# Performance work log

Measured on AMD Instinct MI355X. Metric: run time of the kernel, lower is better.

The kernel has to match this reference:

```python
import jax, jax.numpy as jnp
import numpy as np

B, N, K, D, H, FF, L, NH = 8, 50, 20, 3, 128, 2048, 3, 8
S = N * K
HD = H // NH


def setup_inputs() -> dict:
    key = jax.random.key(0)
    ks = jax.random.split(key, 16)
    visited = jax.random.uniform(ks[0], (B, S)) < 0.05
    # the single most-recent action per batch row (status flips 0 -> 1)
    action_idx = jax.random.randint(ks[1], (B,), 0, S)
    visited = visited.at[jnp.arange(B), action_idx].set(True)
    feats = jax.random.normal(ks[2], (B, S, D - 1)) * visited[:, :, None]
    state = jnp.concatenate([feats, visited[:, :, None].astype(jnp.float32)], axis=-1)
    prev_state = state.at[jnp.arange(B), action_idx, :].set(0.0)

    def w(k, shape, s=0.02):
        return jax.random.normal(k, shape, dtype=jnp.float32) * s

    return dict(
        prev_state=prev_state, state=state,
        W_pre=w(ks[3], (D, H)), b_pre=jnp.zeros(H),
        Wq=w(ks[4], (L, H, H)), bq=jnp.zeros((L, H)),
        Wk=w(ks[5], (L, H, H)), bk=jnp.zeros((L, H)),
        Wv=w(ks[6], (L, H, H)), bv=jnp.zeros((L, H)),
        Wo=w(ks[7], (L, H, H)), bo=jnp.zeros((L, H)),
        ln1_g=jnp.ones((L, H)), ln1_b=jnp.zeros((L, H)),
        Wff1=w(ks[8], (L, H, FF)), bff1=jnp.zeros((L, FF)),
        Wff2=w(ks[9], (L, FF, H)), bff2=jnp.zeros((L, H)),
        ln2_g=jnp.ones((L, H)), ln2_b=jnp.zeros((L, H)),
        W_comb=w(ks[10], (2 * H, H)), b_comb=jnp.zeros(H),
        W_dec=w(ks[11], (H, H)), b_dec=jnp.zeros(H),
        W_lin=w(ks[12], (S, S)), b_lin=jnp.zeros(S),
    )


def _layer_norm(x, g, b, eps=1e-5):
    m = jnp.mean(x, -1, keepdims=True)
    v = jnp.mean(jnp.square(x - m), -1, keepdims=True)
    return (x - m) * jax.lax.rsqrt(v + eps) * g + b


def _update_mask(state):
    # vectorized equivalent of the original Python-loop scatter mask
    status = state[:, :, -1] != 0                      # visited [B, S], S = K*N channel-major
    mask = status
    vis_kn = status.reshape(B, K, N)
    user_any = vis_kn.any(axis=1)                      # [B, N]: user visited on any channel
    mask = mask | jnp.broadcast_to(user_any[:, None, :], (B, K, N)).reshape(B, S)
    assigned = state.reshape(B, K, N, D).sum(-1) != 0  # [B, K, N]
    full = assigned.sum(-1) >= 2                       # [B, K]: channel already has 2 users
    mask = mask | jnp.broadcast_to(full[:, :, None], (B, K, N)).reshape(B, S)
    return mask


def reference(prev_state, state, W_pre, b_pre, Wq, bq, Wk, bk, Wv, bv, Wo, bo,
              ln1_g, ln1_b, Wff1, bff1, Wff2, bff2, ln2_g, ln2_b,
              W_comb, b_comb, W_dec, b_dec, W_lin, b_lin):
    mask = _update_mask(state)
    # exactly one status change per batch row (sequential RL step)
    diff = prev_state[:, :, -1] != state[:, :, -1]
    act_idx = jnp.argmax(diff, axis=1)                 # [B]

    x = state @ W_pre + b_pre                          # [B, S, H]
    scale = np.float32(1.0 / np.sqrt(HD))
    for i in range(L):  # 3 post-LN transformer encoder layers
        q = (x @ Wq[i] + bq[i]).reshape(B, S, NH, HD)
        k = (x @ Wk[i] + bk[i]).reshape(B, S, NH, HD)
        v = (x @ Wv[i] + bv[i]).reshape(B, S, NH, HD)
        att = jax.nn.softmax(jnp.einsum('bqhd,bkhd->bhqk', q, k) * scale, axis=-1)
        o = jnp.einsum('bhqk,bkhd->bqhd', att, v).reshape(B, S, H) @ Wo[i] + bo[i]
        x = _layer_norm(x + o, ln1_g[i], ln1_b[i])
        ff = jax.nn.relu(x @ Wff1[i] + bff1[i]) @ Wff2[i] + bff2[i]
        x = _layer_norm(x + ff, ln2_g[i], ln2_b[i])

    last = x[jnp.arange(B), act_idx]                   # [B, H]
    combined = jnp.concatenate([x.mean(axis=1), last], axis=-1)  # [B, 2H]
    g = combined @ W_comb + b_comb                     # [B, H]
    dec = x @ W_dec + b_dec                            # [B, S, H]
    scores = jnp.einsum('bsh,bh->bs', dec, g)          # [B, S]
    masked = scores @ W_lin + b_lin                    # Q-Learning head
    return jnp.where(mask, -jnp.inf, masked)
```

## Files before the change

kernel.cpp:

```cpp
#include <hip/hip_runtime.h>
#include <math.h>

#define Bb 8
#define Ss 1000
#define Kk 20
#define Nn 50
#define Dd 3
#define Hh 128
#define FFf 2048
#define Ll 3
#define NHh 8
#define HDd 16
#define ROWS (Bb*Ss)

#define SENTINEL -3.0e38f

typedef unsigned short ush;
typedef short short8 __attribute__((ext_vector_type(8)));
typedef float f32x4 __attribute__((ext_vector_type(4)));

__device__ __forceinline__ ush f2b(float f) {
  unsigned x = __float_as_uint(f);
  return (ush)((x + 0x7fff + ((x >> 16) & 1)) >> 16);
}

__global__ __launch_bounds__(256) void mask_kernel(const float* __restrict__ state,
                                                   const float* __restrict__ prev_state,
                                                   int* __restrict__ mask, int* __restrict__ act_idx) {
  int b = blockIdx.x, tid = threadIdx.x;
  __shared__ unsigned char status[Ss], assigned[Ss], uany[Nn], fullk[Kk];
  __shared__ int act;
  if (tid == 0) act = 1 << 30;
  __syncthreads();
  for (int s = tid; s < Ss; s += 256) {
    const float* st = state + ((size_t)b * Ss + s) * Dd;
    float f2 = st[2];
    status[s] = (f2 != 0.f);
    assigned[s] = ((st[0] + st[1] + f2) != 0.f);
    float p2 = prev_state[((size_t)b * Ss + s) * Dd + 2];
    if (p2 != f2) atomicMin(&act, s);
  }
  __syncthreads();
  if (tid < Nn) {
    unsigned char a = 0;
    for (int k = 0; k < Kk; ++k) a |= status[k * Nn + tid];
    uany[tid] = a;
  } else if (tid >= 64 && tid < 64 + Kk) {
    int k = tid - 64, cnt = 0;
    for (int n = 0; n < Nn; ++n) cnt += assigned[k * Nn + n];
    fullk[k] = (cnt >= 2);
  }
  __syncthreads();
  for (int s = tid; s < Ss; s += 256)
    mask[b * Ss + s] = (int)(status[s] | uany[s % Nn] | fullk[s / Nn]);
  if (tid == 0) act_idx[b] = (act >= Ss) ? 0 : act;
}

__global__ __launch_bounds__(256) void pre_kernel(const float* __restrict__ state,
                                                  const float* __restrict__ W_pre,
                                                  const float* __restrict__ b_pre,
                                                  float* __restrict__ x, ush* __restrict__ xbf) {
  int idx = blockIdx.x * 256 + threadIdx.x;
  if (idx >= ROWS * Hh) return;
  int row = idx >> 7, n = idx & 127;
  const float* st = state + (size_t)row * Dd;
  float v = b_pre[n] + st[0] * W_pre[n] + st[1] * W_pre[Hh + n] + st[2] * W_pre[2 * Hh + n];
  x[idx] = v;
  xbf[idx] = f2b(v);
}

#define S1 (384*128)
#define S2 (128*128)
#define S3 (2048*128)
#define S4 (128*2048)
#define SPL (S1+S2+S3+S4)
__global__ __launch_bounds__(256) void wprep_kernel(const float* __restrict__ Wq, const float* __restrict__ Wk,
                                                    const float* __restrict__ Wv, const float* __restrict__ Wo,
                                                    const float* __restrict__ Wff1, const float* __restrict__ Wff2,
                                                    const float* __restrict__ bq, const float* __restrict__ bk,
                                                    const float* __restrict__ bv,
                                                    ush* __restrict__ wqkvT, ush* __restrict__ woT,
                                                    ush* __restrict__ wff1T, ush* __restrict__ wff2T,
                                                    float* __restrict__ bqkv) {
  int idx = blockIdx.x * 256 + threadIdx.x;
  if (idx < Ll * SPL) {
    int l = idx / SPL, r = idx % SPL;
    if (r < S1) {
      int k = r / 384, n = r % 384;
      float v = (n < 128) ? Wq[((size_t)l * Hh + k) * Hh + n]
              : (n < 256) ? Wk[((size_t)l * Hh + k) * Hh + (n - 128)]
                          : Wv[((size_t)l * Hh + k) * Hh + (n - 256)];
      wqkvT[((size_t)l * 384 + n) * 128 + k] = f2b(v);
    } else if (r < S1 + S2) {
      int rr = r - S1; int k = rr >> 7, n = rr & 127;
      woT[((size_t)l * 128 + n) * 128 + k] = f2b(Wo[((size_t)l * Hh + k) * Hh + n]);
    } else if (r < S1 + S2 + S3) {
      int rr = r - S1 - S2; int k = rr >> 11, n = rr & 2047;
      wff1T[((size_t)l * 2048 + n) * 128 + k] = f2b(Wff1[((size_t)l * Hh + k) * FFf + n]);
    } else {
      int rr = r - S1 - S2 - S3; int k = rr >> 7, n = rr & 127;
      wff2T[((size_t)l * 128 + n) * 2048 + k] = f2b(Wff2[((size_t)l * FFf + k) * Hh + n]);
    }
  }
  if (idx < Ll * 384) {
    int l = idx / 384, c = idx % 384;
    bqkv[idx] = (c < 128) ? bq[l * Hh + c] : (c < 256 ? bk[l * Hh + c - 128] : bv[l * Hh + c - 256]);
  }
}

#define LDP 40
template <int ABF16, int OBF16, int RELU, int PARTIAL>
__global__ __launch_bounds__(256) void gemm_mfma(const void* __restrict__ A, const ush* __restrict__ Wt,
                                                 const float* __restrict__ bias, void* __restrict__ out,
                                                 int M, int N, int K, int klen) {
  __shared__ ush As[64 * LDP];
  __shared__ ush Bs[64 * LDP];
  int tid = threadIdx.x;
  int lane = tid & 63, wid = tid >> 6;
  int wr = wid >> 1, wc = wid & 1;
  int m0 = blockIdx.y * 64, n0 = blockIdx.x * 64;
  int lrow = tid >> 2, lk = (tid & 3) << 3;
  int quad = lane >> 4, l16 = lane & 15, kb = quad << 3;
  int kstart = PARTIAL ? blockIdx.z * klen : 0;

  f32x4 acc[2][2];
#pragma unroll
  for (int i = 0; i < 2; ++i)
#pragma unroll
    for (int j = 0; j < 2; ++j) acc[i][j] = (f32x4){0.f, 0.f, 0.f, 0.f};

  for (int k0 = kstart; k0 < kstart + klen; k0 += 32) {
    if (ABF16) {
      short8 av = *(const short8*)((const ush*)A + (size_t)(m0 + lrow) * K + k0 + lk);
      *(short8*)&As[lrow * LDP + lk] = av;
    } else {
      const float* ap = (const float*)A + (size_t)(m0 + lrow) * K + k0 + lk;
      short8 s;
#pragma unroll
      for (int i = 0; i < 8; ++i) s[i] = (short)f2b(ap[i]);
      *(short8*)&As[lrow * LDP + lk] = s;
    }
    short8 bv = *(const short8*)&Wt[(size_t)(n0 + lrow) * K + k0 + lk];
    *(short8*)&Bs[lrow * LDP + lk] = bv;
    __syncthreads();

    short8 a0 = *(short8*)&As[(wr * 32 + l16) * LDP + kb];
    short8 a1 = *(short8*)&As[(wr * 32 + 16 + l16) * LDP + kb];
    short8 b0 = *(short8*)&Bs[(wc * 32 + l16) * LDP + kb];
    short8 b1 = *(short8*)&Bs[(wc * 32 + 16 + l16) * LDP + kb];
    acc[0][0] = __builtin_amdgcn_mfma_f32_16x16x32_bf16(a0, b0, acc[0][0], 0, 0, 0);
    acc[0][1] = __builtin_amdgcn_mfma_f32_16x16x32_bf16(a0, b1, acc[0][1], 0, 0, 0);
    acc[1][0] = __builtin_amdgcn_mfma_f32_16x16x32_bf16(a1, b0, acc[1][0], 0, 0, 0);
    acc[1][1] = __builtin_amdgcn_mfma_f32_16x16x32_bf16(a1, b1, acc[1][1], 0, 0, 0);
    __syncthreads();
  }

  float* pout = PARTIAL ? ((float*)out + (size_t)blockIdx.z * M * N) : (float*)out;
#pragma unroll
  for (int i = 0; i < 2; ++i)
#pragma unroll
    for (int j = 0; j < 2; ++j) {
      int col = n0 + wc * 32 + j * 16 + l16;
      int rbase = m0 + wr * 32 + i * 16 + quad * 4;
      float bval = (!PARTIAL || blockIdx.z == 0) ? bias[col] : 0.f;
#pragma unroll
      for (int v = 0; v < 4; ++v) {
        float o = acc[i][j][v] + bval;
        if (RELU) o = fmaxf(o, 0.f);
        if (OBF16) ((ush*)out)[(size_t)(rbase + v) * N + col] = f2b(o);
        else       pout[(size_t)(rbase + v) * N + col] = o;
      }
    }
}

__global__ __launch_bounds__(256) void attn_mfma(const ush* __restrict__ qkv,
                                                 ush* __restrict__ attn_o) {
  int blk = blockIdx.x;
  int local = blk >> 3;
  int bh = ((blk & 7) << 3) | (local >> 4);
  int qt = local & 15;
  int b = bh >> 3, h = bh & 7;
  int qbase = qt * 64;
  int tid = threadIdx.x, lane = tid & 63, w = tid >> 6;
  int l16 = lane & 15, quad = lane >> 4, kb = quad * 8;

  __shared__ ush Ks[64][40];
  __shared__ ush Vs[16][72];
  __shared__ ush Pb[4][16][72];

  if (tid < 128) {
    *(short8*)&Ks[tid >> 1][16 + (tid & 1) * 8] = (short8){0, 0, 0, 0, 0, 0, 0, 0};
  }

  int qrow = qbase + w * 16 + l16; if (qrow >= Ss) qrow = Ss - 1;
  short8 aq = *(const short8*)(qkv + (size_t)(b * Ss + qrow) * 384 + h * HDd + kb);

  const short one_b = (short)0x3F80;
  const short8 ones = (short8){one_b, one_b, one_b, one_b, one_b, one_b, one_b, one_b};
  f32x4 acc_pv = (f32x4){0.f, 0.f, 0.f, 0.f};
  f32x4 acc_l = (f32x4){0.f, 0.f, 0.f, 0.f};
  const f32x4 zero4 = (f32x4){0.f, 0.f, 0.f, 0.f};

  for (int k0 = 0; k0 < Ss; k0 += 64) {
    __syncthreads();
    if (tid < 128) {
      int row = tid >> 1, g = tid & 1;
      int key = k0 + row;
      short8 s8 = (short8){0, 0, 0, 0, 0, 0, 0, 0};
      if (key < Ss)
        s8 = *(const short8*)(qkv + (size_t)(b * Ss + key) * 384 + 128 + h * HDd + g * 8);
      *(short8*)&Ks[row][g * 8] = s8;
    }
    {
      int d = tid & 15, kg = tid >> 4;
#pragma unroll
      for (int i = 0; i < 4; ++i) {
        int key = k0 + kg * 4 + i;
        Vs[d][kg * 4 + i] = (key < Ss)
            ? qkv[(size_t)(b * Ss + key) * 384 + 256 + h * HDd + d] : (ush)0;
      }
    }
    __syncthreads();

#pragma unroll
    for (int kn = 0; kn < 4; ++kn) {
      short8 bk = *(short8*)&Ks[kn * 16 + l16][kb];
      f32x4 s = __builtin_amdgcn_mfma_f32_16x16x32_bf16(aq, bk, zero4, 0, 0, 0);
      int key = k0 + kn * 16 + l16;
      float m = (key < Ss) ? 1.f : 0.f;
#pragma unroll
      for (int r = 0; r < 4; ++r)
        Pb[w][quad * 4 + r][kn * 16 + l16] = f2b(__expf(s[r] * 0.25f) * m);
    }
    short8 pa0 = *(short8*)&Pb[w][l16][kb];
    short8 pa1 = *(short8*)&Pb[w][l16][32 + kb];
    short8 vb0 = *(short8*)&Vs[l16][kb];
    short8 vb1 = *(short8*)&Vs[l16][32 + kb];
    acc_pv = __builtin_amdgcn_mfma_f32_16x16x32_bf16(pa0, vb0, acc_pv, 0, 0, 0);
    acc_pv = __builtin_amdgcn_mfma_f32_16x16x32_bf16(pa1, vb1, acc_pv, 0, 0, 0);
    acc_l = __builtin_amdgcn_mfma_f32_16x16x32_bf16(pa0, ones, acc_l, 0, 0, 0);
    acc_l = __builtin_amdgcn_mfma_f32_16x16x32_bf16(pa1, ones, acc_l, 0, 0, 0);
  }

#pragma unroll
  for (int r = 0; r < 4; ++r) {
    int q = qbase + w * 16 + quad * 4 + r;
    if (q < Ss)
      attn_o[((size_t)(b * Ss + q)) * Hh + h * HDd + l16] = f2b(acc_pv[r] / acc_l[r]);
  }
}

__global__ __launch_bounds__(128) void resid_ln_kernel(float* __restrict__ x, ush* __restrict__ xbf,
                                                       const float* __restrict__ r, int nparts, size_t pstride,
                                                       const float* __restrict__ g, const float* __restrict__ bb) {
  int row = blockIdx.x, n = threadIdx.x;
  float v = x[(size_t)row * Hh + n];
  for (int p = 0; p < nparts; ++p) v += r[p * pstride + (size_t)row * Hh + n];
  float s = v;
  for (int off = 32; off; off >>= 1) s += __shfl_down(s, off);
  __shared__ float red[2], red2[2];
  int wid = n >> 6;
  if ((n & 63) == 0) red[wid] = s;
  __syncthreads();
  float mean = (red[0] + red[1]) * (1.f / Hh);
  float d = v - mean;
  float s2 = d * d;
  for (int off = 32; off; off >>= 1) s2 += __shfl_down(s2, off);
  if ((n & 63) == 0) red2[wid] = s2;
  __syncthreads();
  float var = (red2[0] + red2[1]) * (1.f / Hh);
  float o = d * rsqrtf(var + 1e-5f) * g[n] + bb[n];
  x[(size_t)row * Hh + n] = o;
  xbf[(size_t)row * Hh + n] = f2b(o);
}

__global__ __launch_bounds__(128) void mean_part_kernel(const float* __restrict__ x,
                                                        float* __restrict__ mpart) {
  int c = blockIdx.x, b = blockIdx.y, n = threadIdx.x;
  const float* xb = x + ((size_t)b * Ss + c * 125) * Hh + n;
  float s = 0.f;
#pragma unroll 5
  for (int i = 0; i < 125; ++i) s += xb[(size_t)i * Hh];
  mpart[(c * Bb + b) * Hh + n] = s;
}

__global__ __launch_bounds__(128) void ghc_kernel(const float* __restrict__ x, const float* __restrict__ mpart,
                                                  const int* __restrict__ act_idx,
                                                  const float* __restrict__ W_comb, const float* __restrict__ b_comb,
                                                  const float* __restrict__ W_dec, const float* __restrict__ b_dec,
                                                  float* __restrict__ h, float* __restrict__ cb) {
  int b = blockIdx.x, n = threadIdx.x;
  __shared__ float cs[2 * Hh], gs[Hh], red[2];
  float mean = 0.f;
#pragma unroll
  for (int c = 0; c < 8; ++c) mean += mpart[(c * Bb + b) * Hh + n];
  cs[n] = mean * (1.f / Ss);
  cs[Hh + n] = x[((size_t)b * Ss + act_idx[b]) * Hh + n];
  __syncthreads();
  float acc = b_comb[n];
  for (int j = 0; j < 2 * Hh; ++j) acc += cs[j] * W_comb[(size_t)j * Hh + n];
  gs[n] = acc;
  __syncthreads();
  float hv = 0.f;
  for (int c = 0; c < Hh; ++c) hv += W_dec[(size_t)n * Hh + c] * gs[c];
  h[b * Hh + n] = hv;
  float t = b_dec[n] * gs[n];
  for (int off = 32; off; off >>= 1) t += __shfl_down(t, off);
  if ((n & 63) == 0) red[n >> 6] = t;
  __syncthreads();
  if (n == 0) cb[b] = red[0] + red[1];
}

__global__ __launch_bounds__(256) void scores_kernel(const float* __restrict__ x, const float* __restrict__ h,
                                                     const float* __restrict__ cb, float* __restrict__ scores) {
  int wid = threadIdx.x >> 6, lane = threadIdx.x & 63;
  int row = blockIdx.x * 4 + wid;
  if (row >= ROWS) return;
  int b = row / Ss;
  const float* xr = x + (size_t)row * Hh;
  const float* hb = h + b * Hh;
  float s = xr[lane] * hb[lane] + xr[lane + 64] * hb[lane + 64];
  for (int off = 32; off; off >>= 1) s += __shfl_down(s, off);
  if (lane == 0) scores[row] = s + cb[b];
}

__global__ __launch_bounds__(256) void final_part(const float* __restrict__ scores,
                                                  const float* __restrict__ W_lin,
                                                  float* __restrict__ fpart) {
  int spc = blockIdx.x, kc = blockIdx.y, b = blockIdx.z;
  int tid = threadIdx.x;
  __shared__ float ss[125];
  for (int i = tid; i < 125; i += 256) ss[i] = scores[b * Ss + kc * 125 + i];
  __syncthreads();
  if (tid < 250) {
    int sp = spc * 250 + tid;
    float acc = 0.f;
    const float* wl = &W_lin[(size_t)(kc * 125) * Ss + sp];
#pragma unroll 5
    for (int s = 0; s < 125; ++s) acc = fmaf(ss[s], wl[(size_t)s * Ss], acc);
    fpart[((size_t)kc * Bb + b) * Ss + sp] = acc;
  }
}

__global__ __launch_bounds__(256) void final_combine(const float* __restrict__ fpart,
                                                     const float* __restrict__ b_lin,
                                                     const int* __restrict__ mask,
                                                     float* __restrict__ out) {
  int b = blockIdx.y;
  int sp = blockIdx.x * 256 + threadIdx.x;
  if (sp >= Ss) return;
  float acc = b_lin[sp];
#pragma unroll
  for (int kc = 0; kc < 8; ++kc) acc += fpart[((size_t)kc * Bb + b) * Ss + sp];
  out[b * Ss + sp] = mask[b * Ss + sp] ? SENTINEL : acc;
}

extern "C" void kernel_launch(void* const* d_in, const int* in_sizes, int n_in,
                              void* d_out, int out_size, void* d_ws, size_t ws_size,
                              hipStream_t stream) {
  const float* prev_state = (const float*)d_in[0];
  const float* state = (const float*)d_in[1];
  const float* W_pre = (const float*)d_in[2];
  const float* b_pre = (const float*)d_in[3];
  const float* Wq = (const float*)d_in[4];
  const float* bq = (const float*)d_in[5];
  const float* Wk = (const float*)d_in[6];
  const float* bk = (const float*)d_in[7];
  const float* Wv = (const float*)d_in[8];
  const float* bv = (const float*)d_in[9];
  const float* Wo = (const float*)d_in[10];
  const float* bo = (const float*)d_in[11];
  const float* ln1_g = (const float*)d_in[12];
  const float* ln1_b = (const float*)d_in[13];
  const float* Wff1 = (const float*)d_in[14];
  const float* bff1 = (const float*)d_in[15];
  const float* Wff2 = (const float*)d_in[16];
  const float* bff2 = (const float*)d_in[17];
  const float* ln2_g = (const float*)d_in[18];
  const float* ln2_b = (const float*)d_in[19];
  const float* W_comb = (const float*)d_in[20];
  const float* b_comb = (const float*)d_in[21];
  const float* W_dec = (const float*)d_in[22];
  const float* b_dec = (const float*)d_in[23];
  const float* W_lin = (const float*)d_in[24];
  const float* b_lin = (const float*)d_in[25];

  char* wsp = (char*)d_ws;
  auto alloc = [&](size_t bytes) { char* p = wsp; wsp += (bytes + 255) & ~(size_t)255; return p; };
  int* mask = (int*)alloc(ROWS * 4);
  int* act = (int*)alloc(Bb * 4);
  ush* wqkvT = (ush*)alloc((size_t)Ll * 384 * 128 * 2);
  ush* woT = (ush*)alloc((size_t)Ll * 128 * 128 * 2);
  ush* wff1T = (ush*)alloc((size_t)Ll * 2048 * 128 * 2);
  ush* wff2T = (ush*)alloc((size_t)Ll * 128 * 2048 * 2);
  float* bqkv = (float*)alloc((size_t)Ll * 384 * 4);
  float* x = (float*)alloc((size_t)ROWS * Hh * 4);
  ush* xbf = (ush*)alloc((size_t)ROWS * Hh * 2);
  float* tmp = (float*)alloc((size_t)ROWS * Hh * 4);
  ush* qkv_bf = (ush*)alloc((size_t)ROWS * 384 * 2);
  ush* attn_ob = (ush*)alloc((size_t)ROWS * Hh * 2);
  float* ff2p = (float*)alloc((size_t)4 * ROWS * Hh * 4);
  float* mpart = (float*)alloc((size_t)8 * Bb * Hh * 4);
  float* hbuf = (float*)alloc((size_t)Bb * Hh * 4);
  float* cb = (float*)alloc((size_t)Bb * 4);
  float* scores = (float*)alloc((size_t)ROWS * 4);
  float* fpart = (float*)alloc((size_t)8 * Bb * Ss * 4);
  ush* ffb = (ush*)alloc((size_t)ROWS * FFf * 2);

  wprep_kernel<<<dim3((Ll * SPL + 255) / 256), 256, 0, stream>>>(Wq, Wk, Wv, Wo, Wff1, Wff2, bq, bk, bv,
                                                                 wqkvT, woT, wff1T, wff2T, bqkv);
  mask_kernel<<<Bb, 256, 0, stream>>>(state, prev_state, mask, act);
  pre_kernel<<<dim3((ROWS * Hh + 255) / 256), 256, 0, stream>>>(state, W_pre, b_pre, x, xbf);

  for (int l = 0; l < Ll; ++l) {
    gemm_mfma<1, 1, 0, 0><<<dim3(384 / 64, ROWS / 64), 256, 0, stream>>>(
        xbf, wqkvT + (size_t)l * 384 * 128, bqkv + l * 384, qkv_bf, ROWS, 384, 128, 128);
    attn_mfma<<<dim3(16 * Bb * NHh), 256, 0, stream>>>(qkv_bf, attn_ob);
    gemm_mfma<1, 0, 0, 0><<<dim3(128 / 64, ROWS / 64), 256, 0, stream>>>(
        attn_ob, woT + (size_t)l * 128 * 128, bo + l * Hh, tmp, ROWS, 128, 128, 128);
    resid_ln_kernel<<<ROWS, 128, 0, stream>>>(x, xbf, tmp, 1, 0, ln1_g + l * Hh, ln1_b + l * Hh);
    gemm_mfma<1, 1, 1, 0><<<dim3(2048 / 64, ROWS / 64), 256, 0, stream>>>(
        xbf, wff1T + (size_t)l * 2048 * 128, bff1 + l * FFf, ffb, ROWS, 2048, 128, 128);
    gemm_mfma<1, 0, 0, 1><<<dim3(128 / 64, ROWS / 64, 4), 256, 0, stream>>>(
        ffb, wff2T + (size_t)l * 128 * 2048, bff2 + l * Hh, ff2p, ROWS, 128, 2048, 512);
    resid_ln_kernel<<<ROWS, 128, 0, stream>>>(x, xbf, ff2p, 4, (size_t)ROWS * Hh, ln2_g + l * Hh, ln2_b + l * Hh);
  }

  mean_part_kernel<<<dim3(8, Bb), 128, 0, stream>>>(x, mpart);
  ghc_kernel<<<Bb, 128, 0, stream>>>(x, mpart, act, W_comb, b_comb, W_dec, b_dec, hbuf, cb);
  scores_kernel<<<dim3(ROWS / 4), 256, 0, stream>>>(x, hbuf, cb, scores);
  final_part<<<dim3(4, 8, Bb), 256, 0, stream>>>(scores, W_lin, fpart);
  final_combine<<<dim3(4, Bb), 256, 0, stream>>>(fpart, b_lin, mask, (float*)d_out);
}
```

Measured before the change: 436.9 us.

## Fuse Wo projection with residual LayerNorm, double query tiles per attention block

Adds a wo_ln_kernel that computes the attention output projection for 64 rows by the full 128 columns and applies bias, the residual add and LayerNorm in-register. This removes the tmp round trip and one launch per layer. Attention blocks now process 128 queries, two 64-row sub-tiles sharing each staged K/V tile, halving K/V reloads but halving grid size to 512 blocks. The second resid_ln kernel now handles two rows per 256-thread block; the fused LN uses the single-pass E[x^2]-mean^2 variance, which is slightly less numerically robust.

```diff
diff --git a/kernel.cpp b/kernel.cpp
--- a/kernel.cpp
+++ b/kernel.cpp
@@ -173,14 +173,90 @@
     }
 }
 
+#define WLP 132
+__global__ __launch_bounds__(256) void wo_ln_kernel(const ush* __restrict__ A, const ush* __restrict__ Wt,
+                                                    const float* __restrict__ bias,
+                                                    const float* __restrict__ ln_g, const float* __restrict__ ln_b,
+                                                    float* __restrict__ x, ush* __restrict__ xbf) {
+  __shared__ char smem[64 * WLP * 4];
+  ush* As = (ush*)smem;
+  ush* Bs = As + 64 * LDP;
+  float* xs = (float*)smem;
+  __shared__ float pbias[128], pg[128], pb2[128];
+
+  int tid = threadIdx.x, lane = tid & 63, w = tid >> 6;
+  int l16 = lane & 15, quad = lane >> 4, kb = quad * 8;
+  int m0 = blockIdx.x * 64;
+  if (tid < 128) { pbias[tid] = bias[tid]; pg[tid] = ln_g[tid]; pb2[tid] = ln_b[tid]; }
+
+  f32x4 acc[8];
+#pragma unroll
+  for (int j = 0; j < 8; ++j) acc[j] = (f32x4){0.f, 0.f, 0.f, 0.f};
+
+  int srow = tid >> 2, slk = (tid & 3) << 3;
+  for (int k0 = 0; k0 < 128; k0 += 32) {
+    *(short8*)&As[srow * LDP + slk] = *(const short8*)(A + (size_t)(m0 + srow) * 128 + k0 + slk);
+#pragma unroll
+    for (int rr = 0; rr < 2; ++rr) {
+      int row = rr * 64 + srow;
+      *(short8*)&Bs[row * LDP + slk] = *(const short8*)(Wt + (size_t)row * 128 + k0 + slk);
+    }
+    __syncthreads();
+    short8 aA = *(short8*)&As[(w * 16 + l16) * LDP + kb];
+#pragma unroll
+    for (int j = 0; j < 8; ++j) {
+      short8 bj = *(short8*)&Bs[(j * 16 + l16) * LDP + kb];
+      acc[j] = __builtin_amdgcn_mfma_f32_16x16x32_bf16(aA, bj, acc[j], 0, 0, 0);
+    }
+    __syncthreads();
+  }
+
+  for (int e = tid; e < 64 * 32; e += 256) {
+    int idx = e * 4; int row = idx >> 7, col = idx & 127;
+    *(float4*)&xs[row * WLP + col] = *(const float4*)&x[(size_t)(m0 + row) * 128 + col];
+  }
+  __syncthreads();
+
+  float v[8][4], s1[4] = {0.f, 0.f, 0.f, 0.f}, s2[4] = {0.f, 0.f, 0.f, 0.f};
+#pragma unroll
+  for (int j = 0; j < 8; ++j) {
+    int col = j * 16 + l16;
+#pragma unroll
+    for (int r = 0; r < 4; ++r) {
+      int rowt = w * 16 + quad * 4 + r;
+      float vv = acc[j][r] + pbias[col] + xs[rowt * WLP + col];
+      v[j][r] = vv; s1[r] += vv; s2[r] += vv * vv;
+    }
+  }
+#pragma unroll
+  for (int m = 1; m <= 8; m <<= 1) {
+#pragma unroll
+    for (int r = 0; r < 4; ++r) { s1[r] += __shfl_xor(s1[r], m); s2[r] += __shfl_xor(s2[r], m); }
+  }
+#pragma unroll
+  for (int r = 0; r < 4; ++r) {
+    int rowt = w * 16 + quad * 4 + r;
+    float mean = s1[r] * (1.f / 128.f);
+    float var = s2[r] * (1.f / 128.f) - mean * mean;
+    float rstd = rsqrtf(var + 1e-5f);
+#pragma unroll
+    for (int j = 0; j < 8; ++j) {
+      int col = j * 16 + l16;
+      float o = (v[j][r] - mean) * rstd * pg[col] + pb2[col];
+      size_t gi = (size_t)(m0 + rowt) * 128 + col;
+      x[gi] = o; xbf[gi] = f2b(o);
+    }
+  }
+}
+
 __global__ __launch_bounds__(256) void attn_mfma(const ush* __restrict__ qkv,
                                                  ush* __restrict__ attn_o) {
   int blk = blockIdx.x;
   int local = blk >> 3;
-  int bh = ((blk & 7) << 3) | (local >> 4);
-  int qt = local & 15;
+  int bh = ((blk & 7) << 3) | (local >> 3);
+  int qt = local & 7;
   int b = bh >> 3, h = bh & 7;
-  int qbase = qt * 64;
+  int qbase = qt * 128;
   int tid = threadIdx.x, lane = tid & 63, w = tid >> 6;
   int l16 = lane & 15, quad = lane >> 4, kb = quad * 8;
 
@@ -188,17 +264,20 @@
   __shared__ ush Vs[16][72];
   __shared__ ush Pb[4][16][72];
 
-  if (tid < 128) {
+  if (tid < 128)
     *(short8*)&Ks[tid >> 1][16 + (tid & 1) * 8] = (short8){0, 0, 0, 0, 0, 0, 0, 0};
-  }
-
-  int qrow = qbase + w * 16 + l16; if (qrow >= Ss) qrow = Ss - 1;
-  short8 aq = *(const short8*)(qkv + (size_t)(b * Ss + qrow) * 384 + h * HDd + kb);
+
+  short8 aq[2];
+#pragma unroll
+  for (int s = 0; s < 2; ++s) {
+    int qrow = qbase + s * 64 + w * 16 + l16; if (qrow >= Ss) qrow = Ss - 1;
+    aq[s] = *(const short8*)(qkv + (size_t)(b * Ss + qrow) * 384 + h * HDd + kb);
+  }
 
   const short one_b = (short)0x3F80;
   const short8 ones = (short8){one_b, one_b, one_b, one_b, one_b, one_b, one_b, one_b};
-  f32x4 acc_pv = (f32x4){0.f, 0.f, 0.f, 0.f};
-  f32x4 acc_l = (f32x4){0.f, 0.f, 0.f, 0.f};
+  f32x4 acc_pv[2] = {(f32x4){0.f, 0.f, 0.f, 0.f}, (f32x4){0.f, 0.f, 0.f, 0.f}};
+  f32x4 acc_l[2] = {(f32x4){0.f, 0.f, 0.f, 0.f}, (f32x4){0.f, 0.f, 0.f, 0.f}};
   const f32x4 zero4 = (f32x4){0.f, 0.f, 0.f, 0.f};
 
   for (int k0 = 0; k0 < Ss; k0 += 64) {
@@ -222,53 +301,60 @@
     }
     __syncthreads();
 
-#pragma unroll
-    for (int kn = 0; kn < 4; ++kn) {
-      short8 bk = *(short8*)&Ks[kn * 16 + l16][kb];
-      f32x4 s = __builtin_amdgcn_mfma_f32_16x16x32_bf16(aq, bk, zero4, 0, 0, 0);
-      int key = k0 + kn * 16 + l16;
-      float m = (key < Ss) ? 1.f : 0.f;
-#pragma unroll
-      for (int r = 0; r < 4; ++r)
-        Pb[w][quad * 4 + r][kn * 16 + l16] = f2b(__expf(s[r] * 0.25f) * m);
-    }
-    short8 pa0 = *(short8*)&Pb[w][l16][kb];
-    short8 pa1 = *(short8*)&Pb[w][l16][32 + kb];
     short8 vb0 = *(short8*)&Vs[l16][kb];
     short8 vb1 = *(short8*)&Vs[l16][32 + kb];
-    acc_pv = __builtin_amdgcn_mfma_f32_16x16x32_bf16(pa0, vb0, acc_pv, 0, 0, 0);
-    acc_pv = __builtin_amdgcn_mfma_f32_16x16x32_bf16(pa1, vb1, acc_pv, 0, 0, 0);
-    acc_l = __builtin_amdgcn_mfma_f32_16x16x32_bf16(pa0, ones, acc_l, 0, 0, 0);
-    acc_l = __builtin_amdgcn_mfma_f32_16x16x32_bf16(pa1, ones, acc_l, 0, 0, 0);
-  }
-
-#pragma unroll
-  for (int r = 0; r < 4; ++r) {
-    int q = qbase + w * 16 + quad * 4 + r;
-    if (q < Ss)
-      attn_o[((size_t)(b * Ss + q)) * Hh + h * HDd + l16] = f2b(acc_pv[r] / acc_l[r]);
-  }
-}
-
-__global__ __launch_bounds__(128) void resid_ln_kernel(float* __restrict__ x, ush* __restrict__ xbf,
+#pragma unroll
+    for (int s = 0; s < 2; ++s) {
+#pragma unroll
+      for (int kn = 0; kn < 4; ++kn) {
+        short8 bk = *(short8*)&Ks[kn * 16 + l16][kb];
+        f32x4 sc = __builtin_amdgcn_mfma_f32_16x16x32_bf16(aq[s], bk, zero4, 0, 0, 0);
+        int key = k0 + kn * 16 + l16;
+        float m = (key < Ss) ? 1.f : 0.f;
+#pragma unroll
+        for (int r = 0; r < 4; ++r)
+          Pb[w][quad * 4 + r][kn * 16 + l16] = f2b(__expf(sc[r] * 0.25f) * m);
+      }
+      short8 pa0 = *(short8*)&Pb[w][l16][kb];
+      short8 pa1 = *(short8*)&Pb[w][l16][32 + kb];
+      acc_pv[s] = __builtin_amdgcn_mfma_f32_16x16x32_bf16(pa0, vb0, acc_pv[s], 0, 0, 0);
+      acc_pv[s] = __builtin_amdgcn_mfma_f32_16x16x32_bf16(pa1, vb1, acc_pv[s], 0, 0, 0);
+      acc_l[s] = __builtin_amdgcn_mfma_f32_16x16x32_bf16(pa0, ones, acc_l[s], 0, 0, 0);
+      acc_l[s] = __builtin_amdgcn_mfma_f32_16x16x32_bf16(pa1, ones, acc_l[s], 0, 0, 0);
+    }
+  }
+
+#pragma unroll
+  for (int s = 0; s < 2; ++s)
+#pragma unroll
+    for (int r = 0; r < 4; ++r) {
+      int q = qbase + s * 64 + w * 16 + quad * 4 + r;
+      if (q < Ss)
+        attn_o[((size_t)(b * Ss + q)) * Hh + h * HDd + l16] = f2b(acc_pv[s][r] / acc_l[s][r]);
+    }
+}
+
+__global__ __launch_bounds__(256) void resid_ln_kernel(float* __restrict__ x, ush* __restrict__ xbf,
                                                        const float* __restrict__ r, int nparts, size_t pstride,
                                                        const float* __restrict__ g, const float* __restrict__ bb) {
-  int row = blockIdx.x, n = threadIdx.x;
+  int half = threadIdx.x >> 7;
+  int row = blockIdx.x * 2 + half;
+  int n = threadIdx.x & 127;
+  int wid = threadIdx.x >> 6;
   float v = x[(size_t)row * Hh + n];
   for (int p = 0; p < nparts; ++p) v += r[p * pstride + (size_t)row * Hh + n];
   float s = v;
   for (int off = 32; off; off >>= 1) s += __shfl_down(s, off);
-  __shared__ float red[2], red2[2];
-  int wid = n >> 6;
-  if ((n & 63) == 0) red[wid] = s;
-  __syncthreads();
-  float mean = (red[0] + red[1]) * (1.f / Hh);
+  __shared__ float red[4], red2[4];
+  if ((threadIdx.x & 63) == 0) red[wid] = s;
+  __syncthreads();
+  float mean = (red[half * 2] + red[half * 2 + 1]) * (1.f / Hh);
   float d = v - mean;
   float s2 = d * d;
   for (int off = 32; off; off >>= 1) s2 += __shfl_down(s2, off);
-  if ((n & 63) == 0) red2[wid] = s2;
-  __syncthreads();
-  float var = (red2[0] + red2[1]) * (1.f / Hh);
+  if ((threadIdx.x & 63) == 0) red2[wid] = s2;
+  __syncthreads();
+  float var = (red2[half * 2] + red2[half * 2 + 1]) * (1.f / Hh);
   float o = d * rsqrtf(var + 1e-5f) * g[n] + bb[n];
   x[(size_t)row * Hh + n] = o;
   xbf[(size_t)row * Hh + n] = f2b(o);
@@ -396,7 +482,6 @@
   float* bqkv = (float*)alloc((size_t)Ll * 384 * 4);
   float* x = (float*)alloc((size_t)ROWS * Hh * 4);
   ush* xbf = (ush*)alloc((size_t)ROWS * Hh * 2);
-  float* tmp = (float*)alloc((size_t)ROWS * Hh * 4);
   ush* qkv_bf = (ush*)alloc((size_t)ROWS * 384 * 2);
   ush* attn_ob = (ush*)alloc((size_t)ROWS * Hh * 2);
   float* ff2p = (float*)alloc((size_t)4 * ROWS * Hh * 4);
@@ -415,15 +500,14 @@
   for (int l = 0; l < Ll; ++l) {
     gemm_mfma<1, 1, 0, 0><<<dim3(384 / 64, ROWS / 64), 256, 0, stream>>>(
         xbf, wqkvT + (size_t)l * 384 * 128, bqkv + l * 384, qkv_bf, ROWS, 384, 128, 128);
-    attn_mfma<<<dim3(16 * Bb * NHh), 256, 0, stream>>>(qkv_bf, attn_ob);
-    gemm_mfma<1, 0, 0, 0><<<dim3(128 / 64, ROWS / 64), 256, 0, stream>>>(
-        attn_ob, woT + (size_t)l * 128 * 128, bo + l * Hh, tmp, ROWS, 128, 128, 128);
-    resid_ln_kernel<<<ROWS, 128, 0, stream>>>(x, xbf, tmp, 1, 0, ln1_g + l * Hh, ln1_b + l * Hh);
+    attn_mfma<<<dim3(512), 256, 0, stream>>>(qkv_bf, attn_ob);
+    wo_ln_kernel<<<dim3(ROWS / 64), 256, 0, stream>>>(
+        attn_ob, woT + (size_t)l * 128 * 128, bo + l * Hh, ln1_g + l * Hh, ln1_b + l * Hh, x, xbf);
     gemm_mfma<1, 1, 1, 0><<<dim3(2048 / 64, ROWS / 64), 256, 0, stream>>>(
         xbf, wff1T + (size_t)l * 2048 * 128, bff1 + l * FFf, ffb, ROWS, 2048, 128, 128);
     gemm_mfma<1, 0, 0, 1><<<dim3(128 / 64, ROWS / 64, 4), 256, 0, stream>>>(
         ffb, wff2T + (size_t)l * 128 * 2048, bff2 + l * Hh, ff2p, ROWS, 128, 2048, 512);
-    resid_ln_kernel<<<ROWS, 128, 0, stream>>>(x, xbf, ff2p, 4, (size_t)ROWS * Hh, ln2_g + l * Hh, ln2_b + l * Hh);
+    resid_ln_kernel<<<ROWS / 2, 256, 0, stream>>>(x, xbf, ff2p, 4, (size_t)ROWS * Hh, ln2_g + l * Hh, ln2_b + l * Hh);
   }
 
   mean_part_kernel<<<dim3(8, Bb), 128, 0, stream>>>(x, mpart);
```

Measured after the change: 468.4 us. +7.2%, slower.
